# Kernel tuning notes

Measured on AMD Instinct MI355X. Metric: run time of the kernel, lower is better.

Reference implementation:

```python
import jax, jax.numpy as jnp
import numpy as np

D_MODEL = 1024
N_HEADS = 16
D_KV = 64
NUM_BUCKETS = 32
MAX_DISTANCE = 128


def _relative_position_bucket(seq_len, num_buckets=NUM_BUCKETS, max_distance=MAX_DISTANCE):
    # bidirectional=True path of T5 bucketing
    ctx = jnp.arange(seq_len, dtype=jnp.int32)[:, None]
    mem = jnp.arange(seq_len, dtype=jnp.int32)[None, :]
    rel = mem - ctx  # [S, S]
    nb = num_buckets // 2
    buckets = (rel > 0).astype(jnp.int32) * nb
    rel = jnp.abs(rel)
    max_exact = nb // 2
    is_small = rel < max_exact
    # guard log(0); those entries are overridden by is_small anyway
    rel_f = jnp.maximum(rel, 1).astype(jnp.float32)
    rel_large = max_exact + (
        jnp.log(rel_f / max_exact) / np.log(max_distance / max_exact) * (nb - max_exact)
    ).astype(jnp.int32)
    rel_large = jnp.minimum(rel_large, nb - 1)
    return buckets + jnp.where(is_small, rel, rel_large)  # [S, S] int32


def setup_inputs() -> dict:
    key = jax.random.key(0)
    ks = jax.random.split(key, 11)
    B, S = 4, 2048
    hidden_states = jax.random.normal(ks[0], (B, S, D_MODEL), dtype=jnp.float32)
    attention_masks = jnp.zeros((B, 1, S, S), dtype=jnp.float32)
    w = lambda k: jax.random.normal(k, (D_MODEL, D_MODEL), dtype=jnp.float32) * 0.02
    b = lambda k: jax.random.normal(k, (D_MODEL,), dtype=jnp.float32) * 0.02
    rel_emb = jax.random.normal(ks[9], (NUM_BUCKETS, N_HEADS), dtype=jnp.float32) * 0.02
    return {
        "hidden_states": hidden_states,
        "attention_masks": attention_masks,
        "Wq": w(ks[1]), "bq": b(ks[2]),
        "Wk": w(ks[3]), "bk": b(ks[4]),
        "Wv": w(ks[5]), "bv": b(ks[6]),
        "Wo": w(ks[7]), "bo": b(ks[8]),
        "rel_emb": rel_emb,
    }


def reference(hidden_states, attention_masks, Wq, bq, Wk, bk, Wv, bv, Wo, bo, rel_emb):
    B, S, _ = hidden_states.shape

    def shape_heads(x):  # [B,S,D] -> [B,H,S,dk]
        return x.reshape(B, S, N_HEADS, D_KV).transpose(0, 2, 1, 3)

    q = shape_heads(hidden_states @ Wq.T + bq)
    k = shape_heads(hidden_states @ Wk.T + bk)
    v = shape_heads(hidden_states @ Wv.T + bv)

    scores = jnp.einsum("bhqd,bhkd->bhqk", q, k)  # [B,H,S,S]

    buckets = _relative_position_bucket(S)  # [S,S]
    position_bias = rel_emb[buckets].transpose(2, 0, 1)[None]  # [1,H,S,S]
    masks = position_bias + attention_masks  # broadcast -> [B,H,S,S]
    scores = scores + masks

    # NOTE: original scales by d_kv**2 (not sqrt), after mask addition
    attn = jax.nn.softmax(scores / float(D_KV ** 2), axis=-1)

    out = jnp.einsum("bhqk,bhkd->bhqd", attn, v)
    out = out.transpose(0, 2, 1, 3).reshape(B, S, D_MODEL)
    out = out @ Wo.T + bo
    return (out, masks)
```

## Files before the change

kernel.cpp:

```cpp
#include <hip/hip_runtime.h>
#include <cmath>


typedef __attribute__((ext_vector_type(8))) short bf16x8;
typedef __attribute__((ext_vector_type(4))) float f32x4;
typedef __attribute__((ext_vector_type(8))) unsigned short u16x8;

#define MFMA16(a, b, c) __builtin_amdgcn_mfma_f32_16x16x32_bf16((a), (b), (c), 0, 0, 0)

#define ASYNC_COPY16(g, l)                                                              \
  __builtin_amdgcn_global_load_lds((const __attribute__((address_space(1))) void*)(g),  \
                                   (__attribute__((address_space(3))) void*)(l), 16, 0, 0)

__device__ __forceinline__ unsigned short f2bf(float f) {
  unsigned u = __float_as_uint(f);
  u += 0x7FFFu + ((u >> 16) & 1u);
  return (unsigned short)(u >> 16);
}
__device__ __forceinline__ float bf2f(unsigned short u) {
  return __uint_as_float(((unsigned)u) << 16);
}

__device__ __forceinline__ int t5_bucket(int rel) {
  int bkt = (rel > 0) ? 16 : 0;
  int d = (rel < 0) ? -rel : rel;
  int v;
  if (d < 8) v = d;
  else if (d < 12) v = 8;
  else if (d < 16) v = 9;
  else if (d < 23) v = 10;
  else if (d < 32) v = 11;
  else if (d < 46) v = 12;
  else if (d < 64) v = 13;
  else if (d < 91) v = 14;
  else v = 15;
  return bkt + v;
}

struct Cast5Args {
  const float* src[5];
  unsigned short* dst[5];
};
__global__ __launch_bounds__(256) void cast5_kernel(Cast5Args a) {
  int i = (blockIdx.x * 256 + threadIdx.x) * 4;
  int seg, loc;
  if (i < 8388608) { seg = 0; loc = i; }
  else { seg = 1 + ((i - 8388608) >> 20); loc = (i - 8388608) & 1048575; }
  float4 v = *(const float4*)(a.src[seg] + loc);
  ushort4 o;
  o.x = f2bf(v.x); o.y = f2bf(v.y); o.z = f2bf(v.z); o.w = f2bf(v.w);
  *(ushort4*)(a.dst[seg] + loc) = o;
}

__device__ __forceinline__ void gemm_core(const unsigned short* __restrict__ A,
                                          const unsigned short* __restrict__ Bt,
                                          const float* __restrict__ bias,
                                          void* __restrict__ Cout, int M, int N, int K,
                                          int epi, short* As, short* Bs) {
  const int lane = threadIdx.x & 63;
  const int wave = threadIdx.x >> 6;
  const int l15 = lane & 15, g = lane >> 4;
  const int m0 = blockIdx.x * 128;
  const int n0 = blockIdx.y * 128;
  const int wr = wave >> 1, wc = wave & 1;

  f32x4 acc[4][4] = {};

  const int srow_in = lane >> 3;
  const int spu = lane & 7;

  for (int k0 = 0; k0 < K; k0 += 64) {
#pragma unroll
    for (int q = 0; q < 4; ++q) {
      const int rbase = (wave * 4 + q) * 8;
      const int row = rbase + srow_in;
      const int usrc = spu ^ (row & 7);
      ASYNC_COPY16(A + (size_t)(m0 + row) * K + k0 + usrc * 8, As + rbase * 64);
      ASYNC_COPY16(Bt + (size_t)(n0 + row) * K + k0 + usrc * 8, Bs + rbase * 64);
    }
    __syncthreads();

#pragma unroll
    for (int kk = 0; kk < 2; ++kk) {
      bf16x8 af[4], bfr[4];
#pragma unroll
      for (int mi = 0; mi < 4; ++mi) {
        int row = wr * 64 + mi * 16 + l15;
        int pu = (kk * 4 + g) ^ (row & 7);
        af[mi] = *(const bf16x8*)(As + row * 64 + pu * 8);
      }
#pragma unroll
      for (int ni = 0; ni < 4; ++ni) {
        int row = wc * 64 + ni * 16 + l15;
        int pu = (kk * 4 + g) ^ (row & 7);
        bfr[ni] = *(const bf16x8*)(Bs + row * 64 + pu * 8);
      }
#pragma unroll
      for (int mi = 0; mi < 4; ++mi)
#pragma unroll
        for (int ni = 0; ni < 4; ++ni)
          acc[mi][ni] = MFMA16(af[mi], bfr[ni], acc[mi][ni]);
    }
    __syncthreads();
  }

  float bvv[4];
#pragma unroll
  for (int ni = 0; ni < 4; ++ni) bvv[ni] = bias[n0 + wc * 64 + ni * 16 + l15];

#pragma unroll
  for (int mi = 0; mi < 4; ++mi) {
    int rbase = m0 + wr * 64 + mi * 16 + (g << 2);
#pragma unroll
    for (int ni = 0; ni < 4; ++ni) {
      int col = n0 + wc * 64 + ni * 16 + l15;
#pragma unroll
      for (int r = 0; r < 4; ++r) {
        float x = acc[mi][ni][r] + bvv[ni];
        if (epi == 0) {
          ((float*)Cout)[(size_t)(rbase + r) * N + col] = x;
        } else if (epi == 1) {
          ((unsigned short*)Cout)[(size_t)(rbase + r) * N + col] = f2bf(x);
        } else {
          int m = rbase + r;
          ((unsigned short*)Cout)[((size_t)((m >> 11) * 1024 + col) << 11) + (m & 2047)] =
              f2bf(x);
        }
      }
    }
  }
}

struct QKVArgs {
  const unsigned short* A;
  const unsigned short* Bt[3];
  const float* bias[3];
  unsigned short* out[3];
};
__global__ __launch_bounds__(256) void qkv_gemm(QKVArgs a) {
  __shared__ __align__(16) short As[128 * 64];
  __shared__ __align__(16) short Bs[128 * 64];
  const int z = blockIdx.z;
  gemm_core(a.A, a.Bt[z], a.bias[z], a.out[z], 8192, 1024, 1024, z == 2 ? 2 : 1, As, Bs);
}

__global__ __launch_bounds__(256) void gemm_f32(const unsigned short* A,
                                                const unsigned short* Bt, const float* bias,
                                                float* Cout) {
  __shared__ __align__(16) short As[128 * 64];
  __shared__ __align__(16) short Bs[128 * 64];
  gemm_core(A, Bt, bias, Cout, 8192, 1024, 1024, 0, As, Bs);
}

template <int WM>
__global__ __launch_bounds__(512) void attn_fused(const unsigned short* __restrict__ Qg,
                                                  const unsigned short* __restrict__ Kg,
                                                  const unsigned short* __restrict__ Vtg,
                                                  const float* __restrict__ am,
                                                  const float* __restrict__ rel_emb,
                                                  unsigned short* __restrict__ Og,
                                                  float* __restrict__ mout) {
  const int bh = blockIdx.x;
  const int b = bh >> 4, h = bh & 15;
  const int q0 = blockIdx.y << 7;
  const int tid = threadIdx.x;
  const int lane = tid & 63, wave = tid >> 6;
  const int l15 = lane & 15, g = lane >> 4;

  __shared__ __align__(16) short Ks[64 * 72];
  __shared__ __align__(16) short Vt[64 * 72];
  __shared__ __align__(16) short Pl[8][16 * 72];
  __shared__ unsigned short pbr[2176];
  __shared__ unsigned short ms[128 * 68];
  short* Qs = (short*)Pl;

  for (int t = tid; t < 2176; t += 512)
    pbr[t] = f2bf(rel_emb[t5_bucket(t - 127 - q0) * 16 + h]);

  const size_t base = ((size_t)b * 2048) * 1024 + h * 64;
  const size_t vtbase = (size_t)bh << 17;

  {
    int row = tid >> 2, cu = (tid & 3) << 4;
    const unsigned short* src = Qg + base + (size_t)(q0 + row) * 1024 + cu;
    u16x8 v0 = *(const u16x8*)src;
    u16x8 v1 = *(const u16x8*)(src + 8);
    *(u16x8*)(Qs + row * 72 + cu) = v0;
    *(u16x8*)(Qs + row * 72 + cu + 8) = v1;
  }
  __syncthreads();

  bf16x8 qf[2];
  {
    int row = (wave << 4) + l15;
    const short* p = Qs + row * 72 + (g << 3);
    qf[0] = *(const bf16x8*)p;
    qf[1] = *(const bf16x8*)(p + 32);
  }

  f32x4 acc[4] = {};
  f32x4 acc1 = {};
  const bf16x8 onesf = {16256, 16256, 16256, 16256, 16256, 16256, 16256, 16256};
  const int ilbase = (wave << 4) + (g << 2);
  const float SC = 1.442695041f / 4096.0f;

  const int srowK = tid >> 3;
  const int scuK = (tid & 7) << 3;
  const int mrow = tid >> 4;
  const int mf4 = tid & 15;

  for (int kt = 0; kt < 32; ++kt) {
    const int j0 = kt << 6;
    __syncthreads();
    {
      const unsigned short* ks = Kg + base + (size_t)(j0 + srowK) * 1024 + scuK;
      *(u16x8*)(Ks + srowK * 72 + scuK) = *(const u16x8*)ks;
      const unsigned short* vs = Vtg + vtbase + ((size_t)srowK << 11) + j0 + scuK;
      *(u16x8*)(Vt + srowK * 72 + scuK) = *(const u16x8*)vs;
    }
    f32x4 mreg[4];
#pragma unroll
    for (int p = 0; p < 4; ++p) {
      const int row = p * 32 + mrow;
      const int j = j0 + (mf4 << 2);
      f32x4 a = *(const f32x4*)(am + ((size_t)b * 2048 + q0 + row) * 2048 + j);
      const int pidx = j - row + 127;
      f32x4 m;
      m[0] = bf2f(pbr[pidx + 0]) + a[0];
      m[1] = bf2f(pbr[pidx + 1]) + a[1];
      m[2] = bf2f(pbr[pidx + 2]) + a[2];
      m[3] = bf2f(pbr[pidx + 3]) + a[3];
      mreg[p] = m;
      ushort4 mb;
      mb.x = f2bf(m[0]); mb.y = f2bf(m[1]); mb.z = f2bf(m[2]); mb.w = f2bf(m[3]);
      *(ushort4*)(ms + row * 68 + (mf4 << 2)) = mb;
    }
    __syncthreads();

    if (WM) {
#pragma unroll
      for (int p = 0; p < 4; ++p) {
        const int row = p * 32 + mrow;
        f32x4* dst =
            (f32x4*)(mout + ((size_t)bh * 2048 + q0 + row) * 2048 + j0 + (mf4 << 2));
        __builtin_nontemporal_store(mreg[p], dst);
      }
    }

    f32x4 sacc[4] = {};
#pragma unroll
    for (int kk = 0; kk < 2; ++kk) {
      const int koff = (kk << 5) + (g << 3);
#pragma unroll
      for (int fj = 0; fj < 4; ++fj) {
        bf16x8 kf = *(const bf16x8*)(Ks + ((fj << 4) + l15) * 72 + koff);
        sacc[fj] = MFMA16(qf[kk], kf, sacc[fj]);
      }
    }

#pragma unroll
    for (int fj = 0; fj < 4; ++fj) {
      const int jl = (fj << 4) + l15;
#pragma unroll
      for (int r = 0; r < 4; ++r) {
        const int il = ilbase + r;
        float mval = bf2f(ms[il * 68 + jl]);
        float p = exp2f((sacc[fj][r] + mval) * SC);
        Pl[wave][((g << 2) + r) * 72 + jl] = (short)f2bf(p);
      }
    }

#pragma unroll
    for (int kk = 0; kk < 2; ++kk) {
      const int koff = (kk << 5) + (g << 3);
      bf16x8 pf = *(const bf16x8*)(&Pl[wave][l15 * 72 + koff]);
      acc1 = MFMA16(pf, onesf, acc1);
#pragma unroll
      for (int fd = 0; fd < 4; ++fd) {
        bf16x8 vf = *(const bf16x8*)(Vt + ((fd << 4) + l15) * 72 + koff);
        acc[fd] = MFMA16(pf, vf, acc[fd]);
      }
    }
  }

#pragma unroll
  for (int fd = 0; fd < 4; ++fd) {
    int d = (fd << 4) + l15;
#pragma unroll
    for (int r = 0; r < 4; ++r) {
      float o = acc[fd][r] / acc1[r];
      Og[base + (size_t)(q0 + ilbase + r) * 1024 + d] = f2bf(o);
    }
  }
}

__global__ __launch_bounds__(256) void masks_kernel(const float* __restrict__ am,
                                                    const float* __restrict__ rel_emb,
                                                    float* __restrict__ mout) {
  const int bi = blockIdx.x;
  const int b = bi >> 11, i = bi & 2047;
  __shared__ float amrow[2048];
  __shared__ float remb[512];
  __shared__ unsigned char bkt[2048];
  for (int t = threadIdx.x; t < 512; t += 256) remb[t] = rel_emb[t];
  const float* arow = am + ((size_t)b * 2048 + i) * 2048;
  for (int t = threadIdx.x; t < 512; t += 256)
    *(float4*)(amrow + (t << 2)) = *(const float4*)(arow + (t << 2));
  for (int j = threadIdx.x; j < 2048; j += 256)
    bkt[j] = (unsigned char)t5_bucket(j - i);
  __syncthreads();
  for (int h = 0; h < 16; ++h) {
    float* dst = mout + (((size_t)(b * 16 + h)) * 2048 + i) * 2048;
    for (int t = threadIdx.x; t < 512; t += 256) {
      int j = t << 2;
      f32x4 o;
      o[0] = remb[(bkt[j + 0] << 4) + h] + amrow[j + 0];
      o[1] = remb[(bkt[j + 1] << 4) + h] + amrow[j + 1];
      o[2] = remb[(bkt[j + 2] << 4) + h] + amrow[j + 2];
      o[3] = remb[(bkt[j + 3] << 4) + h] + amrow[j + 3];
      __builtin_nontemporal_store(o, (f32x4*)(dst + j));
    }
  }
}

extern "C" void kernel_launch(void* const* d_in, const int* in_sizes, int n_in,
                              void* d_out, int out_size, void* d_ws, size_t ws_size,
                              hipStream_t stream) {
  const float* hs  = (const float*)d_in[0];
  const float* am  = (const float*)d_in[1];
  const float* Wq  = (const float*)d_in[2];
  const float* bq  = (const float*)d_in[3];
  const float* Wk  = (const float*)d_in[4];
  const float* bk  = (const float*)d_in[5];
  const float* Wv  = (const float*)d_in[6];
  const float* bv  = (const float*)d_in[7];
  const float* Wo  = (const float*)d_in[8];
  const float* bo  = (const float*)d_in[9];
  const float* rel = (const float*)d_in[10];

  float* out = (float*)d_out;
  float* mout = out + (size_t)8388608;

  const bool fused = ws_size >= (size_t)69206016;

  unsigned short *hsb, *wqb, *wkb, *wvb, *wob, *qb, *kb, *vtb, *aob;
  if (fused) {
    char* W = (char*)d_ws;
    qb  = (unsigned short*)(W);
    kb  = (unsigned short*)(W + 16777216);
    vtb = (unsigned short*)(W + 33554432);
    aob = (unsigned short*)(W + 50331648);
    wob = (unsigned short*)(W + 67108864);
    char* SB = (char*)mout;
    hsb = (unsigned short*)(SB);
    wqb = (unsigned short*)(SB + 16777216);
    wkb = (unsigned short*)(SB + 18874368);
    wvb = (unsigned short*)(SB + 20971520);
  } else {
    char* SB = (char*)mout;
    hsb = (unsigned short*)(SB);
    wqb = (unsigned short*)(SB + 16777216);
    wkb = (unsigned short*)(SB + 18874368);
    wvb = (unsigned short*)(SB + 20971520);
    wob = (unsigned short*)(SB + 23068672);
    qb  = (unsigned short*)(SB + 25165824);
    kb  = (unsigned short*)(SB + 41943040);
    vtb = (unsigned short*)(SB + 58720256);
    aob = (unsigned short*)(SB + 75497472);
  }

  Cast5Args ca;
  ca.src[0] = hs;  ca.dst[0] = hsb;
  ca.src[1] = Wq;  ca.dst[1] = wqb;
  ca.src[2] = Wk;  ca.dst[2] = wkb;
  ca.src[3] = Wv;  ca.dst[3] = wvb;
  ca.src[4] = Wo;  ca.dst[4] = wob;
  cast5_kernel<<<12288, 256, 0, stream>>>(ca);

  QKVArgs qa;
  qa.A = hsb;
  qa.Bt[0] = wqb;  qa.bias[0] = bq;  qa.out[0] = qb;
  qa.Bt[1] = wkb;  qa.bias[1] = bk;  qa.out[1] = kb;
  qa.Bt[2] = wvb;  qa.bias[2] = bv;  qa.out[2] = vtb;
  qkv_gemm<<<dim3(64, 8, 3), 256, 0, stream>>>(qa);

  if (fused) {
    attn_fused<1><<<dim3(64, 16), 512, 0, stream>>>(qb, kb, vtb, am, rel, aob, mout);
  } else {
    attn_fused<0><<<dim3(64, 16), 512, 0, stream>>>(qb, kb, vtb, am, rel, aob, mout);
  }

  gemm_f32<<<dim3(64, 8), 256, 0, stream>>>(aob, wob, bo, out);

  if (!fused) masks_kernel<<<8192, 256, 0, stream>>>(am, rel, mout);
}
```

Before: 456.9 us.

## Stage GEMM epilogue through LDS for coalesced stores; alias mask and P buffers

The bf16 QKV GEMM epilogues now write results into a swizzled shared-memory tile and then emit 16-byte coalesced row stores. This covers both the row-major and the transposed V layouts, replacing scattered 2-byte global stores. In the attention kernel, the mask tile and the per-wave P buffer are merged into one shared array, which cuts LDS use and may raise occupancy. The cost is an extra barrier and an LDS round trip in the epilogue, plus in-place overwrite of mask values with P values.

After: 410.5 us (median of 2 runs). 1.11x faster.

```diff
diff --git a/kernel.cpp b/kernel.cpp
--- a/kernel.cpp
+++ b/kernel.cpp
@@ -56,7 +56,9 @@
                                           const unsigned short* __restrict__ Bt,
                                           const float* __restrict__ bias,
                                           void* __restrict__ Cout, int M, int N, int K,
-                                          int epi, short* As, short* Bs) {
+                                          int epi, short* sh) {
+  short* As = sh;
+  short* Bs = sh + 128 * 64;
   const int lane = threadIdx.x & 63;
   const int wave = threadIdx.x >> 6;
   const int l15 = lane & 15, g = lane >> 4;
@@ -108,24 +110,71 @@
 #pragma unroll
   for (int ni = 0; ni < 4; ++ni) bvv[ni] = bias[n0 + wc * 64 + ni * 16 + l15];
 
-#pragma unroll
-  for (int mi = 0; mi < 4; ++mi) {
-    int rbase = m0 + wr * 64 + mi * 16 + (g << 2);
-#pragma unroll
-    for (int ni = 0; ni < 4; ++ni) {
-      int col = n0 + wc * 64 + ni * 16 + l15;
-#pragma unroll
-      for (int r = 0; r < 4; ++r) {
-        float x = acc[mi][ni][r] + bvv[ni];
-        if (epi == 0) {
-          ((float*)Cout)[(size_t)(rbase + r) * N + col] = x;
-        } else if (epi == 1) {
-          ((unsigned short*)Cout)[(size_t)(rbase + r) * N + col] = f2bf(x);
-        } else {
-          int m = rbase + r;
-          ((unsigned short*)Cout)[((size_t)((m >> 11) * 1024 + col) << 11) + (m & 2047)] =
-              f2bf(x);
+  if (epi == 0) {
+#pragma unroll
+    for (int mi = 0; mi < 4; ++mi) {
+      int rbase = m0 + wr * 64 + mi * 16 + (g << 2);
+#pragma unroll
+      for (int ni = 0; ni < 4; ++ni) {
+        int col = n0 + wc * 64 + ni * 16 + l15;
+#pragma unroll
+        for (int r = 0; r < 4; ++r)
+          ((float*)Cout)[(size_t)(rbase + r) * N + col] = acc[mi][ni][r] + bvv[ni];
+      }
+    }
+  } else if (epi == 1) {
+#pragma unroll
+    for (int mi = 0; mi < 4; ++mi) {
+      int ml = wr * 64 + mi * 16 + (g << 2);
+#pragma unroll
+      for (int ni = 0; ni < 4; ++ni) {
+        int c = wc * 64 + ni * 16 + l15;
+#pragma unroll
+        for (int r = 0; r < 4; ++r) {
+          int m = ml + r;
+          int pc = (((c >> 3) ^ (m & 7)) << 3) | (c & 7);
+          sh[m * 128 + pc] = (short)f2bf(acc[mi][ni][r] + bvv[ni]);
         }
+      }
+    }
+    __syncthreads();
+    {
+      int m = threadIdx.x >> 1, half = threadIdx.x & 1;
+      unsigned short* dst = (unsigned short*)Cout + (size_t)(m0 + m) * N + n0 + half * 64;
+#pragma unroll
+      for (int uu = 0; uu < 8; ++uu) {
+        int u = half * 8 + uu;
+        int pu = u ^ (m & 7);
+        *(u16x8*)(dst + uu * 8) = *(const u16x8*)(sh + m * 128 + pu * 8);
+      }
+    }
+  } else {
+#pragma unroll
+    for (int mi = 0; mi < 4; ++mi) {
+      int ml = wr * 64 + mi * 16 + (g << 2);
+#pragma unroll
+      for (int ni = 0; ni < 4; ++ni) {
+        int c = wc * 64 + ni * 16 + l15;
+#pragma unroll
+        for (int r = 0; r < 4; ++r) {
+          int s = ml + r;
+          int ps = (((s >> 3) ^ (c & 7)) << 3) | (s & 7);
+          sh[c * 128 + ps] = (short)f2bf(acc[mi][ni][r] + bvv[ni]);
+        }
+      }
+    }
+    __syncthreads();
+    {
+      int c = threadIdx.x >> 1, half = threadIdx.x & 1;
+      int col = n0 + c;
+      int mb = m0 >> 11, ml = m0 & 2047;
+      unsigned short* dst =
+          (unsigned short*)Cout + (((size_t)(mb * 1024 + col)) << 11) + ml + half * 64;
+#pragma unroll
+      for (int uu = 0; uu < 8; ++uu) {
+        int u = half * 8 + uu;
+        int pu = u ^ (c & 7);
+        *(u16x8*)(dst + uu * 8) = *(const u16x8*)(sh + c * 128 + pu * 8);
       }
     }
   }
@@ -138,18 +187,16 @@
   unsigned short* out[3];
 };
 __global__ __launch_bounds__(256) void qkv_gemm(QKVArgs a) {
-  __shared__ __align__(16) short As[128 * 64];
-  __shared__ __align__(16) short Bs[128 * 64];
+  __shared__ __align__(16) short sh[2 * 128 * 64];
   const int z = blockIdx.z;
-  gemm_core(a.A, a.Bt[z], a.bias[z], a.out[z], 8192, 1024, 1024, z == 2 ? 2 : 1, As, Bs);
+  gemm_core(a.A, a.Bt[z], a.bias[z], a.out[z], 8192, 1024, 1024, z == 2 ? 2 : 1, sh);
 }
 
 __global__ __launch_bounds__(256) void gemm_f32(const unsigned short* A,
                                                 const unsigned short* Bt, const float* bias,
                                                 float* Cout) {
-  __shared__ __align__(16) short As[128 * 64];
-  __shared__ __align__(16) short Bs[128 * 64];
-  gemm_core(A, Bt, bias, Cout, 8192, 1024, 1024, 0, As, Bs);
+  __shared__ __align__(16) short sh[2 * 128 * 64];
+  gemm_core(A, Bt, bias, Cout, 8192, 1024, 1024, 0, sh);
 }
 
 template <int WM>
@@ -169,10 +216,9 @@
 
   __shared__ __align__(16) short Ks[64 * 72];
   __shared__ __align__(16) short Vt[64 * 72];
-  __shared__ __align__(16) short Pl[8][16 * 72];
   __shared__ unsigned short pbr[2176];
-  __shared__ unsigned short ms[128 * 68];
-  short* Qs = (short*)Pl;
+  __shared__ __align__(16) unsigned short msPl[128 * 72];
+  short* Qs = (short*)msPl;
 
   for (int t = tid; t < 2176; t += 512)
     pbr[t] = f2bf(rel_emb[t5_bucket(t - 127 - q0) * 16 + h]);
@@ -233,7 +279,7 @@
       mreg[p] = m;
       ushort4 mb;
       mb.x = f2bf(m[0]); mb.y = f2bf(m[1]); mb.z = f2bf(m[2]); mb.w = f2bf(m[3]);
-      *(ushort4*)(ms + row * 68 + (mf4 << 2)) = mb;
+      *(ushort4*)(msPl + row * 72 + (mf4 << 2)) = mb;
     }
     __syncthreads();
 
@@ -263,17 +309,17 @@
       const int jl = (fj << 4) + l15;
 #pragma unroll
       for (int r = 0; r < 4; ++r) {
-        const int il = ilbase + r;
-        float mval = bf2f(ms[il * 68 + jl]);
+        const int il = (wave << 4) + (g << 2) + r;
+        float mval = bf2f(msPl[il * 72 + jl]);
         float p = exp2f((sacc[fj][r] + mval) * SC);
-        Pl[wave][((g << 2) + r) * 72 + jl] = (short)f2bf(p);
+        msPl[il * 72 + jl] = f2bf(p);
       }
     }
 
 #pragma unroll
     for (int kk = 0; kk < 2; ++kk) {
       const int koff = (kk << 5) + (g << 3);
-      bf16x8 pf = *(const bf16x8*)(&Pl[wave][l15 * 72 + koff]);
+      bf16x8 pf = *(const bf16x8*)((const short*)msPl + ((wave << 4) + l15) * 72 + koff);
       acc1 = MFMA16(pf, onesf, acc1);
 #pragma unroll
       for (int fd = 0; fd < 4; ++fd) {
```
